# Kernel optimization log

Measured on AMD Instinct MI355X. Metric: run time of the kernel, lower is better.

## Reference

```python
import jax, jax.numpy as jnp
import numpy as np

B, S, E, P, H, F = 4, 4096, 256, 32, 8, 1024
DH = E // H
LN_EPS = 1e-5


def setup_inputs() -> dict:
    key = jax.random.key(0)
    ks = jax.random.split(key, 12)
    dt = jnp.float32
    return {
        "src": jax.random.normal(ks[0], (B, S, E), dt),
        "pos_embed": jax.random.normal(ks[1], (B, P, S), dt),
        # learnable positional transform (pos_linear: P -> P)
        "Wpos": jax.random.normal(ks[2], (P, P), dt) * (1.0 / np.sqrt(P)),
        "bpos": jnp.zeros((P,), dt),
        # RBF kernel hyperparameters (ScaleKernel(RBFKernel)) -- positive scalars
        "lengthscale": jnp.full((), 2.0, dt),
        "outputscale": jnp.full((), 1.0, dt),
        # value / output projections of multihead attention
        "Wv": jax.random.normal(ks[3], (E, E), dt) * (1.0 / np.sqrt(E)),
        "bv": jnp.zeros((E,), dt),
        "Wo": jax.random.normal(ks[4], (E, E), dt) * (1.0 / np.sqrt(E)),
        "bo": jnp.zeros((E,), dt),
        # feed-forward
        "W1": jax.random.normal(ks[5], (F, E), dt) * (1.0 / np.sqrt(E)),
        "b1": jnp.zeros((F,), dt),
        "W2": jax.random.normal(ks[6], (E, F), dt) * (1.0 / np.sqrt(F)),
        "b2": jnp.zeros((E,), dt),
        # layer norms
        "ln1_g": jnp.ones((E,), dt), "ln1_b": jnp.zeros((E,), dt),
        "ln2_g": jnp.ones((E,), dt), "ln2_b": jnp.zeros((E,), dt),
    }


def _layer_norm(x, g, b):
    mu = jnp.mean(x, -1, keepdims=True)
    var = jnp.mean(jnp.square(x - mu), -1, keepdims=True)
    return (x - mu) * jax.lax.rsqrt(var + LN_EPS) * g + b


def _rbf_scores(x, lengthscale, outputscale):
    # x: [B, S, P] -> scaled RBF kernel matrix [B, S, S]
    xs = x / lengthscale
    sq = jnp.sum(xs * xs, axis=-1)  # [B, S]
    d2 = sq[:, :, None] + sq[:, None, :] - 2.0 * jnp.einsum('bsp,btp->bst', xs, xs)
    d2 = jnp.maximum(d2, 0.0)
    return outputscale * jnp.exp(-0.5 * d2)


def reference(src, pos_embed, Wpos, bpos, lengthscale, outputscale,
              Wv, bv, Wo, bo, W1, b1, W2, b2, ln1_g, ln1_b, ln2_g, ln2_b):
    b, s, e = src.shape
    # learnable positional transform: [B,P,S] -> [B,S,P] -> linear -> back
    pe = jnp.einsum('bps,op->bos', pos_embed, Wpos) + bpos[None, :, None]  # [B,P,S]
    # GP-kernel attention scores over sequence positions
    scores = _rbf_scores(pe.transpose(0, 2, 1), lengthscale, outputscale)  # [B,S,S]
    attn = jax.nn.softmax(scores, axis=-1)
    # value projection, per-head weighted sum (scores shared across heads)
    v = (src @ Wv.T + bv).reshape(b, s, H, DH)
    ctx = jnp.einsum('bqk,bkhd->bqhd', attn, v).reshape(b, s, e)
    attn_out = ctx @ Wo.T + bo
    x = _layer_norm(src + attn_out, ln1_g, ln1_b)
    ff = jax.nn.relu(x @ W1.T + b1) @ W2.T + b2
    return _layer_norm(x + ff, ln2_g, ln2_b)
```

## Files before the change

### kernel.cpp

```cpp
#include <hip/hip_runtime.h>
#include <stdint.h>

#define BN 4
#define SN 4096
#define EN 256
#define PN 32
#define FN 1024
#define BS (BN*SN)
#define PAUG 64

typedef uint16_t bf16_t;
typedef short v4s  __attribute__((ext_vector_type(4)));
typedef short v8s  __attribute__((ext_vector_type(8)));
typedef __bf16 bf16x8 __attribute__((ext_vector_type(8)));
typedef float v4f   __attribute__((ext_vector_type(4)));
typedef float v16f  __attribute__((ext_vector_type(16)));

#define MFMA16(a,b,c) __builtin_amdgcn_mfma_f32_16x16x32_bf16(a,b,c,0,0,0)
#define MFMA32(a,b,c) __builtin_amdgcn_mfma_f32_32x32x16_bf16(a,b,c,0,0,0)

__device__ __forceinline__ float b2f(bf16_t x){
    uint32_t u = ((uint32_t)x) << 16; float f; __builtin_memcpy(&f, &u, 4); return f;
}
__device__ __forceinline__ bf16_t f2b(float f){
    uint32_t u; __builtin_memcpy(&u, &f, 4);
    u += 0x7FFFu + ((u >> 16) & 1u);
    return (bf16_t)(u >> 16);
}
__device__ __forceinline__ bf16x8 ldb8(const bf16_t* p){
    v8s r = *(const v8s*)p; return __builtin_bit_cast(bf16x8, r);
}
__device__ __forceinline__ bf16x8 ldb8u(const bf16_t* p){
    v4s lo = *(const v4s*)p;
    v4s hi = *(const v4s*)(p + 4);
    v8s r = __builtin_shufflevector(lo, hi, 0,1,2,3,4,5,6,7);
    return __builtin_bit_cast(bf16x8, r);
}
__device__ __forceinline__ float ldsc(const float* p){ return *p; }
__device__ __forceinline__ float ldsc(const bf16_t* p){ return b2f(*p); }
__device__ __forceinline__ void stsc(float* p, float v){ *p = v; }
__device__ __forceinline__ void stsc(bf16_t* p, float v){ *p = f2b(v); }

#if __has_builtin(__builtin_amdgcn_exp2f)
__device__ __forceinline__ float fexp2(float x){ return __builtin_amdgcn_exp2f(x); }
#else
__device__ __forceinline__ float fexp2(float x){ return exp2f(x); }
#endif

#if __has_builtin(__builtin_amdgcn_cvt_pk_bf16_f32)
typedef __bf16 bf16x2 __attribute__((ext_vector_type(2)));
__device__ __forceinline__ uint32_t pkbf16(float a, float b){
    bf16x2 r = __builtin_amdgcn_cvt_pk_bf16_f32(a, b);
    return __builtin_bit_cast(uint32_t, r);
}
#else
__device__ __forceinline__ uint32_t pkbf16(float a, float b){
    return (uint32_t)f2b(a) | ((uint32_t)f2b(b) << 16);
}
#endif

typedef const __attribute__((address_space(1))) uint32_t* glds_gp;
typedef __attribute__((address_space(3))) uint32_t* glds_lp;
__device__ __forceinline__ void glds16(const bf16_t* g, bf16_t* l){
    __builtin_amdgcn_global_load_lds((glds_gp)g, (glds_lp)l, 16, 0, 0);
}

__global__ __launch_bounds__(256) void prep_kernel(
    const float* __restrict__ src, bf16_t* __restrict__ srcb,
    const float* __restrict__ Wv, bf16_t* __restrict__ Wvb,
    const float* __restrict__ Wo, bf16_t* __restrict__ Wob,
    const float* __restrict__ W1, bf16_t* __restrict__ W1b,
    const float* __restrict__ W2, bf16_t* __restrict__ W2b,
    const float* __restrict__ pos, const float* __restrict__ Wp,
    const float* __restrict__ bp,  const float* __restrict__ lsp,
    bf16_t* __restrict__ xk, bf16_t* __restrict__ xq)
{
    __shared__ float Wsh[PN*PN];
    __shared__ float bsh[PN];
    int bid = blockIdx.x;
    int tid = threadIdx.x;

    if (bid < 4736){
        const float* sp; bf16_t* dp; int off;
        if (bid < 4096){ sp = src; dp = srcb; off = (bid*256 + tid)*4; }
        else {
            int i = ((bid - 4096)*256 + tid)*4;
            if      (i <  65536){ sp=Wv; dp=Wvb; off=i; }
            else if (i < 131072){
                int idx = i - 65536;
                float4 f = *(const float4*)(Wo + idx);
                v4s o;
                o.x = (short)f2b(f.x); o.y = (short)f2b(f.y);
                o.z = (short)f2b(f.z); o.w = (short)f2b(f.w);
                int n = idx >> 8, k = idx & 255;
                int dst = (((n>>4)*8 + (k>>5))*64 + (((k>>3)&3)*16 + (n&15)))*8 + (k&7);
                *(v4s*)(Wob + dst) = o;
                return;
            }
            else if (i < 393216){ sp=W1; dp=W1b; off=i-131072; }
            else                { sp=W2; dp=W2b; off=i-393216; }
        }
        float4 f = *(const float4*)(sp + off);
        v4s o;
        o.x = (short)f2b(f.x); o.y = (short)f2b(f.y);
        o.z = (short)f2b(f.z); o.w = (short)f2b(f.w);
        *(v4s*)(dp + off) = o;
        return;
    }

    int pb = bid - 4736;
    int b  = pb >> 4;
    int s  = (pb & 15)*256 + tid;

    for (int i = tid; i < PN*PN; i += 256) Wsh[i] = Wp[i];
    if (tid < PN) bsh[tid] = bp[tid];
    __syncthreads();

    float inv_ls = 1.0f / lsp[0];
    const float c1f = 1.4426950408889634f;

    float col[PN];
    #pragma unroll
    for (int p = 0; p < PN; p++) col[p] = pos[((size_t)b*PN + p)*SN + s];

    uint16_t xb[PN], qb[PN];
    float sq = 0.f;
    #pragma unroll 4
    for (int o = 0; o < PN; o++){
        float pe = bsh[o];
        #pragma unroll
        for (int p = 0; p < PN; p++) pe += col[p] * Wsh[o*PN + p];
        float pv = pe * inv_ls;
        uint16_t h = f2b(pv);
        xb[o] = h;
        qb[o] = f2b(c1f * pv);
        float xr = b2f(h);
        sq += xr * xr;
    }

    size_t base = ((size_t)b*SN + s) * PAUG;
    v8s pk[8];
    #pragma unroll
    for (int c = 0; c < 4; c++)
        #pragma unroll
        for (int j = 0; j < 8; j++) ((short*)&pk[c])[j] = (short)xb[c*8 + j];
    #pragma unroll
    for (int c = 4; c < 8; c++)
        #pragma unroll
        for (int j = 0; j < 8; j++) ((short*)&pk[c])[j] = 0;
    ((short*)&pk[4])[0] = (short)f2b(-0.5f * sq);
    ((short*)&pk[4])[1] = (short)0x3F80;
    #pragma unroll
    for (int c = 0; c < 8; c++) *(v8s*)(xk + base + c*8) = pk[c];

    #pragma unroll
    for (int c = 0; c < 4; c++)
        #pragma unroll
        for (int j = 0; j < 8; j++) ((short*)&pk[c])[j] = (short)qb[c*8 + j];
    ((short*)&pk[4])[0] = (short)f2b(c1f);
    ((short*)&pk[4])[1] = (short)f2b(-0.5f * sq * c1f);
    #pragma unroll
    for (int c = 0; c < 8; c++) *(v8s*)(xq + base + c*8) = pk[c];
}

template<int EPI, typename OutT>
__global__ __launch_bounds__(256) void gemm_t(
    const bf16_t* __restrict__ A, const bf16_t* __restrict__ W,
    const float* __restrict__ bias, OutT* __restrict__ out,
    bf16_t* __restrict__ vt, int N, int K)
{
    __shared__ __align__(16) bf16_t At[2][4096];
    __shared__ __align__(16) bf16_t Wt[2][4096];
    int tid = threadIdx.x;
    int lane = tid & 63, wv = tid >> 6, col = lane & 15, quad = lane >> 4;
    int m0 = blockIdx.x * 64, n0 = blockIdx.y * 64;
    int nck = K >> 6;

    int srow = tid >> 3;
    int spc  = (tid & 7) ^ (srow & 7);
    const bf16_t* asrc = A + (size_t)(m0 + srow)*K + spc*8;
    const bf16_t* wsrc = W + (size_t)(n0 + srow)*K + spc*8;

    v4f acc[4];
    #pragma unroll
    for (int t = 0; t < 4; t++) acc[t] = (v4f){0.f,0.f,0.f,0.f};

    glds16(asrc, &At[0][tid*8]);
    glds16(asrc + (size_t)32*K, &At[0][2048 + tid*8]);
    glds16(wsrc, &Wt[0][tid*8]);
    glds16(wsrc + (size_t)32*K, &Wt[0][2048 + tid*8]);
    __syncthreads();

    for (int c = 0; c < nck; c++){
        int cb = c & 1;
        if (c + 1 < nck){
            glds16(asrc + (c+1)*64, &At[cb^1][tid*8]);
            glds16(asrc + (size_t)32*K + (c+1)*64, &At[cb^1][2048 + tid*8]);
            glds16(wsrc + (c+1)*64, &Wt[cb^1][tid*8]);
            glds16(wsrc + (size_t)32*K + (c+1)*64, &Wt[cb^1][2048 + tid*8]);
        }
        #pragma unroll
        for (int kc = 0; kc < 2; kc++){
            int pc = ((kc*4 + quad) ^ (col & 7)) * 8;
            bf16x8 a = ldb8(&At[cb][(wv*16 + col)*64 + pc]);
            #pragma unroll
            for (int t = 0; t < 4; t++){
                bf16x8 b = ldb8(&Wt[cb][(t*16 + col)*64 + pc]);
                acc[t] = MFMA16(a, b, acc[t]);
            }
        }
        __syncthreads();
    }

    float bfv[4];
    #pragma unroll
    for (int t = 0; t < 4; t++) bfv[t] = bias[n0 + t*16 + col];

    if constexpr (EPI == 3){
        __shared__ uint16_t Tsh[64*74];
        #pragma unroll
        for (int r = 0; r < 4; r++)
            #pragma unroll
            for (int t = 0; t < 4; t++)
                Tsh[(wv*16 + quad*4 + r)*74 + t*16 + col] = f2b(acc[t][r] + bfv[t]);
        __syncthreads();
        int e = tid >> 2, sc = tid & 3;
        int b = m0 >> 12;
        int sbat = m0 & (SN-1);
        int eb   = (n0 + e) >> 5;
        int l31e = (n0 + e) & 31;
        int k16  = (sbat >> 4) + sc;
        v8s p0, p1;
        #pragma unroll
        for (int i = 0; i < 8; i++) ((short*)&p0)[i] = (short)Tsh[(sc*16 + i)*74 + e];
        #pragma unroll
        for (int i = 0; i < 8; i++) ((short*)&p1)[i] = (short)Tsh[(sc*16 + 8 + i)*74 + e];
        bf16_t* dst = vt + ((((size_t)b*8 + eb)*256 + k16)*64 + l31e)*8;
        *(v8s*)dst = p0;
        *(v8s*)(dst + 256) = p1;
    } else {
        #pragma unroll
        for (int r = 0; r < 4; r++){
            int row = m0 + wv*16 + quad*4 + r;
            #pragma unroll
            for (int t = 0; t < 4; t++){
                float y = acc[t][r] + bfv[t];
                if constexpr (EPI == 1) y = fmaxf(y, 0.f);
                stsc(out + (size_t)row*N + n0 + t*16 + col, y);
            }
        }
    }
}

template<int EPI>
__global__ __launch_bounds__(256, 2) void gemm128(
    const bf16_t* __restrict__ A, const bf16_t* __restrict__ W,
    const float* __restrict__ bias, bf16_t* __restrict__ out,
    int N, int K)
{
    __shared__ __align__(16) bf16_t At[2][8192];
    __shared__ __align__(16) bf16_t Wt[2][8192];
    int tid = threadIdx.x;
    int lane = tid & 63, wv = tid >> 6, col = lane & 15, quad = lane >> 4;
    int m0 = blockIdx.x * 128, n0 = blockIdx.y * 128;
    int nck = K >> 6;

    int srow = tid >> 3;
    int spc  = (tid & 7) ^ (srow & 7);
    const bf16_t* asrc = A + (size_t)(m0 + srow)*K + spc*8;
    const bf16_t* wsrc = W + (size_t)(n0 + srow)*K + spc*8;

    v4f acc[2][8];
    #pragma unroll
    for (int mi = 0; mi < 2; mi++)
        #pragma unroll
        for (int t = 0; t < 8; t++) acc[mi][t] = (v4f){0.f,0.f,0.f,0.f};

    #pragma unroll
    for (int s = 0; s < 4; s++){
        glds16(asrc + (size_t)(s*32)*K, &At[0][s*2048 + tid*8]);
        glds16(wsrc + (size_t)(s*32)*K, &Wt[0][s*2048 + tid*8]);
    }
    __syncthreads();

    for (int c = 0; c < nck; c++){
        int cb = c & 1;
        if (c + 1 < nck){
            #pragma unroll
            for (int s = 0; s < 4; s++){
                glds16(asrc + (size_t)(s*32)*K + (c+1)*64, &At[cb^1][s*2048 + tid*8]);
                glds16(wsrc + (size_t)(s*32)*K + (c+1)*64, &Wt[cb^1][s*2048 + tid*8]);
            }
        }
        #pragma unroll
        for (int kc = 0; kc < 2; kc++){
            int pc = ((kc*4 + quad) ^ (col & 7)) * 8;
            bf16x8 a[2];
            #pragma unroll
            for (int mi = 0; mi < 2; mi++)
                a[mi] = ldb8(&At[cb][(wv*32 + mi*16 + col)*64 + pc]);
            #pragma unroll
            for (int t = 0; t < 8; t++){
                bf16x8 b = ldb8(&Wt[cb][(t*16 + col)*64 + pc]);
                #pragma unroll
                for (int mi = 0; mi < 2; mi++)
                    acc[mi][t] = MFMA16(a[mi], b, acc[mi][t]);
            }
        }
        __syncthreads();
    }

    float bfv[8];
    #pragma unroll
    for (int t = 0; t < 8; t++) bfv[t] = bias[n0 + t*16 + col];

    #pragma unroll
    for (int mi = 0; mi < 2; mi++){
        #pragma unroll
        for (int r = 0; r < 4; r++){
            int row = m0 + wv*32 + mi*16 + quad*4 + r;
            #pragma unroll
            for (int t = 0; t < 8; t++){
                float y = acc[mi][t][r] + bfv[t];
                if constexpr (EPI == 1) y = fmaxf(y, 0.f);
                out[(size_t)row*N + n0 + t*16 + col] = f2b(y);
            }
        }
    }
}

template<typename OutT>
__global__ __launch_bounds__(512, 4) void gemm_ln(
    const bf16_t* __restrict__ A, const bf16_t* __restrict__ W,
    const float* __restrict__ bias, const bf16_t* __restrict__ res,
    const float* __restrict__ gamma, const float* __restrict__ beta,
    OutT* __restrict__ out, int K)
{
    __shared__ __align__(16) bf16_t At[2][32*64];
    __shared__ __align__(16) bf16_t Wt[2][256*64];
    __shared__ float lnb[4][32][2];

    int tid = threadIdx.x;
    int lane = tid & 63, wv = tid >> 6, col = lane & 15, quad = lane >> 4;
    int mw = wv >> 2;
    int nw = wv & 3;
    int m0 = blockIdx.x * 32;
    int nck = K >> 6;

    int arow = (tid & 255) >> 3;
    int apc  = (tid & 7) ^ (arow & 7);
    const bf16_t* asrc = A + (size_t)(m0 + arow)*K + apc*8;
    int wr0  = tid >> 3;
    const bf16_t* wsrc[4];
    #pragma unroll
    for (int s = 0; s < 4; s++){
        int wrow = s*64 + wr0;
        int wpc  = (tid & 7) ^ (wrow & 7);
        wsrc[s] = W + (size_t)wrow*K + wpc*8;
    }

    v4f acc[4];
    #pragma unroll
    for (int t = 0; t < 4; t++) acc[t] = (v4f){0.f,0.f,0.f,0.f};

    if (tid < 256) glds16(asrc, &At[0][tid*8]);
    #pragma unroll
    for (int s = 0; s < 4; s++) glds16(wsrc[s], &Wt[0][s*4096 + tid*8]);
    __syncthreads();

    for (int c = 0; c < nck; c++){
        int cb = c & 1;
        if (c + 1 < nck){
            if (tid < 256) glds16(asrc + (c+1)*64, &At[cb^1][tid*8]);
            #pragma unroll
            for (int s = 0; s < 4; s++)
                glds16(wsrc[s] + (c+1)*64, &Wt[cb^1][s*4096 + tid*8]);
        }
        #pragma unroll
        for (int kc = 0; kc < 2; kc++){
            int pc = ((kc*4 + quad) ^ (col & 7)) * 8;
            bf16x8 a = ldb8(&At[cb][(mw*16 + col)*64 + pc]);
            #pragma unroll
            for (int t = 0; t < 4; t++){
                bf16x8 b = ldb8(&Wt[cb][(nw*64 + t*16 + col)*64 + pc]);
                acc[t] = MFMA16(a, b, acc[t]);
            }
        }
        __syncthreads();
    }

    float bfv[4];
    #pragma unroll
    for (int t = 0; t < 4; t++) bfv[t] = bias[nw*64 + t*16 + col];

    float v[4][4];
    float s1[4], s2[4];
    #pragma unroll
    for (int r = 0; r < 4; r++){ s1[r] = 0.f; s2[r] = 0.f; }
    #pragma unroll
    for (int r = 0; r < 4; r++){
        int row = m0 + mw*16 + quad*4 + r;
        #pragma unroll
        for (int t = 0; t < 4; t++){
            float x = acc[t][r] + bfv[t]
                    + b2f(res[(size_t)row*EN + nw*64 + t*16 + col]);
            v[t][r] = x; s1[r] += x; s2[r] += x*x;
        }
    }
    #pragma unroll
    for (int r = 0; r < 4; r++){
        #pragma unroll
        for (int m = 1; m <= 8; m <<= 1){
            s1[r] += __shfl_xor(s1[r], m);
            s2[r] += __shfl_xor(s2[r], m);
        }
    }
    if (col == 0){
        #pragma unroll
        for (int r = 0; r < 4; r++){
            int rl = mw*16 + quad*4 + r;
            lnb[nw][rl][0] = s1[r];
            lnb[nw][rl][1] = s2[r];
        }
    }
    __syncthreads();
    #pragma unroll
    for (int r = 0; r < 4; r++){
        int rl  = mw*16 + quad*4 + r;
        int row = m0 + rl;
        float S1 = lnb[0][rl][0] + lnb[1][rl][0] + lnb[2][rl][0] + lnb[3][rl][0];
        float S2 = lnb[0][rl][1] + lnb[1][rl][1] + lnb[2][rl][1] + lnb[3][rl][1];
        float mu = S1 * (1.f/256.f);
        float rs = rsqrtf(S2 * (1.f/256.f) - mu*mu + 1e-5f);
        #pragma unroll
        for (int t = 0; t < 4; t++){
            int gi = nw*64 + t*16 + col;
            stsc(out + (size_t)row*EN + gi, (v[t][r]-mu)*rs*gamma[gi] + beta[gi]);
        }
    }
}

__global__ __launch_bounds__(512, 2) void attn_kernel(
    const bf16_t* __restrict__ xk, const bf16_t* __restrict__ xq,
    const bf16_t* __restrict__ vf, const float* __restrict__ osp,
    const bf16_t* __restrict__ wof, const float* __restrict__ bo,
    const bf16_t* __restrict__ res, const float* __restrict__ gamma,
    const float* __restrict__ beta, bf16_t* __restrict__ out)
{
    __shared__ __align__(16) bf16_t Wtb[2][64*132];
    __shared__ __align__(16) bf16_t Qs[64*64];
    __shared__ __align__(16) bf16_t Osh[64*256];
    __shared__ float densh[8][64];
    __shared__ float dent[64];
    __shared__ float lnw[8][64][2];

    int tid  = threadIdx.x;
    int lane = tid & 63;
    int wv   = tid >> 6;
    int col  = lane & 15;
    int quad = lane >> 4;
    int l31  = lane & 31;
    int half = lane >> 5;

    int bid = blockIdx.x;
    int b   = (bid & 7) >> 1;
    int qi  = ((bid >> 3) << 1) | (bid & 1);
    int q0  = qi * 64;

    float k2 = 1.4426950408889634f * osp[0];

    const bf16_t* xkb = xk + (size_t)b * SN * PAUG;
    const bf16_t* xqb = xq + (size_t)b * SN * PAUG;
    const bf16_t* vfb = vf + (((size_t)b*8 + wv)*256)*512 + lane*8;

    {
        int qrow = tid >> 3;
        int qpc  = (tid & 7) ^ (qrow & 7);
        glds16(xqb + (size_t)(q0 + qrow)*PAUG + qpc*8, &Qs[tid*8]);
    }

    v16f acc[2];
    #pragma unroll
    for (int qg = 0; qg < 2; qg++)
        #pragma unroll
        for (int i = 0; i < 16; i++) acc[qg][i] = 0.f;
    float den[4] = {0.f, 0.f, 0.f, 0.f};
    const v4f zero = (v4f){0.f,0.f,0.f,0.f};

    bf16x8 kf0, kf1;
    {
        const bf16_t* kr = xkb + (size_t)(wv*16 + col)*PAUG + quad*8;
        kf0 = ldb8(kr); kf1 = ldb8(kr + 32);
    }

    __syncthreads();

    for (int c = 0; c < 32; c++){
        int cb = c & 1;
        bf16x8 vr[8];
        #pragma unroll
        for (int sk = 0; sk < 8; sk++)
            vr[sk] = ldb8(vfb + (size_t)(c*8 + sk)*512);

        #pragma unroll
        for (int qg = 0; qg < 2; qg++){
            #pragma unroll
            for (int g2 = 0; g2 < 2; g2++){
                int qr = qg*32 + g2*16 + col;
                bf16x8 qa = ldb8(&Qs[qr*64 + ((quad    ) ^ (col & 7))*8]);
                bf16x8 qb = ldb8(&Qs[qr*64 + ((4 + quad) ^ (col & 7))*8]);
                v4f st = MFMA16(kf0, qa, zero);
                st = MFMA16(kf1, qb, st);
                #pragma unroll
                for (int rp = 0; rp < 2; rp++){
                    float w0 = fexp2(fmaf(k2, fexp2(st[rp*2+0]), -k2));
                    float w1 = fexp2(fmaf(k2, fexp2(st[rp*2+1]), -k2));
                    den[qg*2+g2] += w0 + w1;
                    *(uint32_t*)&Wtb[cb][qr*132 + wv*16 + quad*4 + rp*2]
                        = pkbf16(w0, w1);
                }
            }
        }

        if (c + 1 < 32){
            const bf16_t* kr = xkb + (size_t)((c+1)*128 + wv*16 + col)*PAUG + quad*8;
            kf0 = ldb8(kr); kf1 = ldb8(kr + 32);
        }

        asm volatile("s_waitcnt lgkmcnt(0)" ::: "memory");
        __builtin_amdgcn_s_barrier();
        __builtin_amdgcn_sched_barrier(0);

        #pragma unroll
        for (int qg = 0; qg < 2; qg++){
            #pragma unroll
            for (int sk4 = 0; sk4 < 2; sk4++){
                bf16x8 af[4];
                #pragma unroll
                for (int j = 0; j < 4; j++)
                    af[j] = ldb8u(&Wtb[cb][(qg*32 + l31)*132 + (sk4*4 + j)*16 + half*8]);
                #pragma unroll
                for (int j = 0; j < 4; j++)
                    acc[qg] = MFMA32(af[j], vr[sk4*4 + j], acc[qg]);
            }
        }
    }

    #pragma unroll
    for (int d = 0; d < 4; d++){
        den[d] += __shfl_xor(den[d], 16);
        den[d] += __shfl_xor(den[d], 32);
    }
    if (lane < 16){
        #pragma unroll
        for (int qg = 0; qg < 2; qg++)
            #pragma unroll
            for (int g2 = 0; g2 < 2; g2++)
                densh[wv][qg*32 + g2*16 + lane] = den[qg*2+g2];
    }
    __syncthreads();
    if (tid < 64){
        float s = 0.f;
        #pragma unroll
        for (int w = 0; w < 8; w++) s += densh[w][tid];
        dent[tid] = 1.f / s;
    }
    __syncthreads();

    #pragma unroll
    for (int qg = 0; qg < 2; qg++){
        #pragma unroll
        for (int rg = 0; rg < 16; rg++){
            int qrow = qg*32 + (rg & 3) + 8*(rg >> 2) + 4*half;
            int e = wv*32 + l31;
            int g = e >> 3;
            Osh[qrow*256 + ((g ^ (qrow & 7))*8) + (e & 7)] = f2b(acc[qg][rg] * dent[qrow]);
        }
    }
    __syncthreads();

    v4f y[4][2];
    #pragma unroll
    for (int qg = 0; qg < 4; qg++)
        #pragma unroll
        for (int t = 0; t < 2; t++) y[qg][t] = (v4f){0.f,0.f,0.f,0.f};

    #pragma unroll
    for (int kc = 0; kc < 8; kc++){
        bf16x8 b0 = ldb8(wof + (size_t)(((wv*2+0)*8 + kc)*64 + lane)*8);
        bf16x8 b1 = ldb8(wof + (size_t)(((wv*2+1)*8 + kc)*64 + lane)*8);
        #pragma unroll
        for (int qg = 0; qg < 4; qg++){
            bf16x8 a = ldb8(&Osh[(qg*16 + col)*256 + (((kc*4 + quad) ^ (col & 7))*8)]);
            y[qg][0] = MFMA16(a, b0, y[qg][0]);
            y[qg][1] = MFMA16(a, b1, y[qg][1]);
        }
    }

    size_t growb = (size_t)b*SN + q0;
    float bo0 = bo[wv*32 + col], bo1 = bo[wv*32 + 16 + col];
    #pragma unroll
    for (int qg = 0; qg < 4; qg++){
        #pragma unroll
        for (int r = 0; r < 4; r++){
            int row = qg*16 + quad*4 + r;
            float x0 = y[qg][0][r] + bo0 + b2f(res[(growb + row)*EN + wv*32 + col]);
            float x1 = y[qg][1][r] + bo1 + b2f(res[(growb + row)*EN + wv*32 + 16 + col]);
            y[qg][0][r] = x0; y[qg][1][r] = x1;
            float s1 = x0 + x1, s2 = x0*x0 + x1*x1;
            #pragma unroll
            for (int m = 1; m <= 8; m <<= 1){
                s1 += __shfl_xor(s1, m);
                s2 += __shfl_xor(s2, m);
            }
            if (col == 0){
                lnw[wv][row][0] = s1;
                lnw[wv][row][1] = s2;
            }
        }
    }
    __syncthreads();

    float g0 = gamma[wv*32 + col],      g1v = gamma[wv*32 + 16 + col];
    float e0 = beta[wv*32 + col],       e1v = beta[wv*32 + 16 + col];
    #pragma unroll
    for (int qg = 0; qg < 4; qg++){
        #pragma unroll
        for (int r = 0; r < 4; r++){
            int row = qg*16 + quad*4 + r;
            float S1 = 0.f, S2 = 0.f;
            #pragma unroll
            for (int w = 0; w < 8; w++){ S1 += lnw[w][row][0]; S2 += lnw[w][row][1]; }
            float mu = S1 * (1.f/256.f);
            float rs = rsqrtf(S2 * (1.f/256.f) - mu*mu + 1e-5f);
            out[(growb + row)*EN + wv*32 + col]      = f2b((y[qg][0][r]-mu)*rs*g0 + e0);
            out[(growb + row)*EN + wv*32 + 16 + col] = f2b((y[qg][1][r]-mu)*rs*g1v + e1v);
        }
    }
}

extern "C" void kernel_launch(void* const* d_in, const int* in_sizes, int n_in,
                              void* d_out, int out_size, void* d_ws, size_t ws_size,
                              hipStream_t stream)
{
    (void)in_sizes; (void)n_in; (void)out_size; (void)ws_size;
    const float* src  = (const float*)d_in[0];
    const float* pos  = (const float*)d_in[1];
    const float* Wpos = (const float*)d_in[2];
    const float* bpos = (const float*)d_in[3];
    const float* ls   = (const float*)d_in[4];
    const float* os   = (const float*)d_in[5];
    const float* Wv   = (const float*)d_in[6];
    const float* bv   = (const float*)d_in[7];
    const float* Wo   = (const float*)d_in[8];
    const float* bo   = (const float*)d_in[9];
    const float* W1   = (const float*)d_in[10];
    const float* b1   = (const float*)d_in[11];
    const float* W2   = (const float*)d_in[12];
    const float* b2   = (const float*)d_in[13];
    const float* g1   = (const float*)d_in[14];
    const float* be1  = (const float*)d_in[15];
    const float* g2   = (const float*)d_in[16];
    const float* be2  = (const float*)d_in[17];

    char* w = (char*)d_ws;
    bf16_t* xkb  = (bf16_t*)(w);
    bf16_t* xqb  = (bf16_t*)(w + ( 2u<<20));
    bf16_t* Wvb  = (bf16_t*)(w + ( 4u<<20));
    bf16_t* Wob  = (bf16_t*)(w + ( 4u<<20) + (1u<<18));
    bf16_t* W1b  = (bf16_t*)(w + ( 5u<<20));
    bf16_t* W2b  = (bf16_t*)(w + ( 6u<<20));
    bf16_t* srcb = (bf16_t*)(w + ( 8u<<20));
    bf16_t* vtg  = (bf16_t*)(w + (16u<<20));
    bf16_t* xws  = (bf16_t*)(w + (24u<<20));
    bf16_t* hws  = (bf16_t*)(w + (32u<<20));

    prep_kernel<<<dim3(4800), 256, 0, stream>>>(
        src, srcb, Wv, Wvb, Wo, Wob, W1, W1b, W2, W2b,
        pos, Wpos, bpos, ls, xkb, xqb);

    gemm_t<3, bf16_t><<<dim3(BS/64, EN/64), 256, 0, stream>>>(
        srcb, Wvb, bv, (bf16_t*)nullptr, vtg, EN, EN);
    attn_kernel<<<dim3(256), 512, 0, stream>>>(
        xkb, xqb, vtg, os, Wob, bo, srcb, g1, be1, xws);
    gemm128<1><<<dim3(BS/128, FN/128), 256, 0, stream>>>(
        xws, W1b, b1, hws, FN, EN);
    gemm_ln<float><<<dim3(BS/32), 512, 0, stream>>>(
        hws, W2b, b2, xws, g2, be2, (float*)d_out, FN);
}
```

Baseline: 231.9 us.

## Fuse FFN up/down GEMMs with LayerNorm and double attention key chunk

Replaces the separate W1 GEMM (writing a bf16 hidden tensor to global memory) and the W2+LayerNorm GEMM with one fused kernel. For each 64-row tile it computes hidden chunks of 64 in LDS and immediately accumulates them into the W2 output, while double-buffering W1/W2 tiles. This removes the global round trip of the hidden activations and one launch, at the cost of fewer blocks (256) and a large LDS footprint. Separately, the attention kernel now processes 256 keys per iteration instead of 128, halving the barrier count but increasing register and LDS pressure.

Measured after the change: 225.6 us. 2.7% less time.

```diff
diff --git a/kernel.cpp b/kernel.cpp
--- a/kernel.cpp
+++ b/kernel.cpp
@@ -252,148 +252,118 @@
     }
 }
 
-template<int EPI>
-__global__ __launch_bounds__(256, 2) void gemm128(
-    const bf16_t* __restrict__ A, const bf16_t* __restrict__ W,
-    const float* __restrict__ bias, bf16_t* __restrict__ out,
-    int N, int K)
+__global__ __launch_bounds__(512) void ffn_ln_kernel(
+    const bf16_t* __restrict__ x,  const bf16_t* __restrict__ W1b,
+    const float* __restrict__ b1,  const bf16_t* __restrict__ W2b,
+    const float* __restrict__ b2,  const float* __restrict__ gamma,
+    const float* __restrict__ beta, float* __restrict__ out)
 {
-    __shared__ __align__(16) bf16_t At[2][8192];
-    __shared__ __align__(16) bf16_t Wt[2][8192];
-    int tid = threadIdx.x;
-    int lane = tid & 63, wv = tid >> 6, col = lane & 15, quad = lane >> 4;
-    int m0 = blockIdx.x * 128, n0 = blockIdx.y * 128;
-    int nck = K >> 6;
-
-    int srow = tid >> 3;
-    int spc  = (tid & 7) ^ (srow & 7);
-    const bf16_t* asrc = A + (size_t)(m0 + srow)*K + spc*8;
-    const bf16_t* wsrc = W + (size_t)(n0 + srow)*K + spc*8;
-
-    v4f acc[2][8];
-    #pragma unroll
-    for (int mi = 0; mi < 2; mi++)
-        #pragma unroll
-        for (int t = 0; t < 8; t++) acc[mi][t] = (v4f){0.f,0.f,0.f,0.f};
-
-    #pragma unroll
-    for (int s = 0; s < 4; s++){
-        glds16(asrc + (size_t)(s*32)*K, &At[0][s*2048 + tid*8]);
-        glds16(wsrc + (size_t)(s*32)*K, &Wt[0][s*2048 + tid*8]);
-    }
-    __syncthreads();
-
-    for (int c = 0; c < nck; c++){
-        int cb = c & 1;
-        if (c + 1 < nck){
-            #pragma unroll
-            for (int s = 0; s < 4; s++){
-                glds16(asrc + (size_t)(s*32)*K + (c+1)*64, &At[cb^1][s*2048 + tid*8]);
-                glds16(wsrc + (size_t)(s*32)*K + (c+1)*64, &Wt[cb^1][s*2048 + tid*8]);
-            }
-        }
-        #pragma unroll
-        for (int kc = 0; kc < 2; kc++){
-            int pc = ((kc*4 + quad) ^ (col & 7)) * 8;
-            bf16x8 a[2];
-            #pragma unroll
-            for (int mi = 0; mi < 2; mi++)
-                a[mi] = ldb8(&At[cb][(wv*32 + mi*16 + col)*64 + pc]);
-            #pragma unroll
-            for (int t = 0; t < 8; t++){
-                bf16x8 b = ldb8(&Wt[cb][(t*16 + col)*64 + pc]);
-                #pragma unroll
-                for (int mi = 0; mi < 2; mi++)
-                    acc[mi][t] = MFMA16(a[mi], b, acc[mi][t]);
-            }
-        }
-        __syncthreads();
-    }
-
-    float bfv[8];
-    #pragma unroll
-    for (int t = 0; t < 8; t++) bfv[t] = bias[n0 + t*16 + col];
-
-    #pragma unroll
-    for (int mi = 0; mi < 2; mi++){
-        #pragma unroll
-        for (int r = 0; r < 4; r++){
-            int row = m0 + wv*32 + mi*16 + quad*4 + r;
-            #pragma unroll
-            for (int t = 0; t < 8; t++){
-                float y = acc[mi][t][r] + bfv[t];
-                if constexpr (EPI == 1) y = fmaxf(y, 0.f);
-                out[(size_t)row*N + n0 + t*16 + col] = f2b(y);
-            }
-        }
-    }
-}
-
-template<typename OutT>
-__global__ __launch_bounds__(512, 4) void gemm_ln(
-    const bf16_t* __restrict__ A, const bf16_t* __restrict__ W,
-    const float* __restrict__ bias, const bf16_t* __restrict__ res,
-    const float* __restrict__ gamma, const float* __restrict__ beta,
-    OutT* __restrict__ out, int K)
-{
-    __shared__ __align__(16) bf16_t At[2][32*64];
-    __shared__ __align__(16) bf16_t Wt[2][256*64];
-    __shared__ float lnb[4][32][2];
-
-    int tid = threadIdx.x;
-    int lane = tid & 63, wv = tid >> 6, col = lane & 15, quad = lane >> 4;
-    int mw = wv >> 2;
-    int nw = wv & 3;
-    int m0 = blockIdx.x * 32;
-    int nck = K >> 6;
-
-    int arow = (tid & 255) >> 3;
-    int apc  = (tid & 7) ^ (arow & 7);
-    const bf16_t* asrc = A + (size_t)(m0 + arow)*K + apc*8;
-    int wr0  = tid >> 3;
-    const bf16_t* wsrc[4];
-    #pragma unroll
-    for (int s = 0; s < 4; s++){
-        int wrow = s*64 + wr0;
-        int wpc  = (tid & 7) ^ (wrow & 7);
-        wsrc[s] = W + (size_t)wrow*K + wpc*8;
-    }
-
-    v4f acc[4];
-    #pragma unroll
-    for (int t = 0; t < 4; t++) acc[t] = (v4f){0.f,0.f,0.f,0.f};
-
-    if (tid < 256) glds16(asrc, &At[0][tid*8]);
-    #pragma unroll
-    for (int s = 0; s < 4; s++) glds16(wsrc[s], &Wt[0][s*4096 + tid*8]);
-    __syncthreads();
-
-    for (int c = 0; c < nck; c++){
-        int cb = c & 1;
-        if (c + 1 < nck){
-            if (tid < 256) glds16(asrc + (c+1)*64, &At[cb^1][tid*8]);
+    __shared__ __align__(16) bf16_t W1c[2][16384];
+    __shared__ __align__(16) bf16_t W2c[2][16384];
+    __shared__ __align__(16) bf16_t Hs[64*68];
+    __shared__ float b1sh[1024];
+    __shared__ float lnb[2][64][2];
+
+    int tid  = threadIdx.x;
+    int lane = tid & 63;
+    int wv   = tid >> 6;
+    int col  = lane & 15;
+    int quad = lane >> 4;
+    int mw   = wv >> 1;
+    int nw   = wv & 1;
+    int m0   = blockIdx.x * 64;
+
+    b1sh[tid]       = b1[tid];
+    b1sh[512 + tid] = b1[512 + tid];
+
+    const bf16_t* xrow = x + (size_t)(m0 + mw*16 + col)*EN + quad*8;
+    bf16x8 xr[8];
+    #pragma unroll
+    for (int kk = 0; kk < 8; kk++) xr[kk] = ldb8(xrow + kk*32);
+
+    float b2v[8], gv[8], bev[8];
+    #pragma unroll
+    for (int t2 = 0; t2 < 8; t2++){
+        int nn = nw*128 + t2*16 + col;
+        b2v[t2] = b2[nn]; gv[t2] = gamma[nn]; bev[t2] = beta[nn];
+    }
+
+    v4f acc[8];
+    #pragma unroll
+    for (int t2 = 0; t2 < 8; t2++) acc[t2] = (v4f){0.f,0.f,0.f,0.f};
+
+    int wr  = tid >> 3;
+    int pp  = tid & 7;
+    int swz = (pp ^ (wr & 7)) * 8;
+
+    #pragma unroll
+    for (int s = 0; s < 4; s++)
+        glds16(W1b + (size_t)wr*256 + s*64 + swz, &W1c[0][s*4096 + tid*8]);
+    #pragma unroll
+    for (int s2 = 0; s2 < 4; s2++)
+        glds16(W2b + (size_t)(s2*64 + wr)*1024 + swz, &W2c[0][s2*4096 + tid*8]);
+
+    #pragma unroll 1
+    for (int c = 0; c < 16; c++){
+        int par = c & 1;
+        if (c < 15){
             #pragma unroll
             for (int s = 0; s < 4; s++)
-                glds16(wsrc[s] + (c+1)*64, &Wt[cb^1][s*4096 + tid*8]);
-        }
-        #pragma unroll
-        for (int kc = 0; kc < 2; kc++){
-            int pc = ((kc*4 + quad) ^ (col & 7)) * 8;
-            bf16x8 a = ldb8(&At[cb][(mw*16 + col)*64 + pc]);
-            #pragma unroll
-            for (int t = 0; t < 4; t++){
-                bf16x8 b = ldb8(&Wt[cb][(nw*64 + t*16 + col)*64 + pc]);
-                acc[t] = MFMA16(a, b, acc[t]);
-            }
-        }
-        __syncthreads();
-    }
-
-    float bfv[4];
-    #pragma unroll
-    for (int t = 0; t < 4; t++) bfv[t] = bias[nw*64 + t*16 + col];
-
-    float v[4][4];
+                glds16(W1b + (size_t)((c+1)*64 + wr)*256 + s*64 + swz,
+                       &W1c[par^1][s*4096 + tid*8]);
+            #pragma unroll
+            for (int s2 = 0; s2 < 4; s2++)
+                glds16(W2b + (size_t)(s2*64 + wr)*1024 + (c+1)*64 + swz,
+                       &W2c[par^1][s2*4096 + tid*8]);
+            asm volatile("s_waitcnt vmcnt(8)" ::: "memory");
+        } else {
+            asm volatile("s_waitcnt vmcnt(0)" ::: "memory");
+        }
+        __builtin_amdgcn_s_barrier();
+        __builtin_amdgcn_sched_barrier(0);
+
+        v4f hacc[2];
+        hacc[0] = (v4f){0.f,0.f,0.f,0.f};
+        hacc[1] = (v4f){0.f,0.f,0.f,0.f};
+        #pragma unroll
+        for (int kk = 0; kk < 8; kk++){
+            #pragma unroll
+            for (int t = 0; t < 2; t++){
+                int hl = nw*32 + t*16 + col;
+                bf16x8 b = ldb8(&W1c[par][(kk>>1)*4096 + hl*64
+                                 + ((((kk&1)*4 + quad) ^ (hl & 7))*8)]);
+                hacc[t] = MFMA16(xr[kk], b, hacc[t]);
+            }
+        }
+        #pragma unroll
+        for (int t = 0; t < 2; t++){
+            float bb = b1sh[c*64 + nw*32 + t*16 + col];
+            #pragma unroll
+            for (int r = 0; r < 4; r++){
+                float h = fmaxf(hacc[t][r] + bb, 0.f);
+                Hs[(mw*16 + quad*4 + r)*68 + nw*32 + t*16 + col] = f2b(h);
+            }
+        }
+        asm volatile("s_waitcnt lgkmcnt(0)" ::: "memory");
+        __builtin_amdgcn_s_barrier();
+        __builtin_amdgcn_sched_barrier(0);
+
+        #pragma unroll
+        for (int kk2 = 0; kk2 < 2; kk2++){
+            bf16x8 a2 = ldb8u(&Hs[(mw*16 + col)*68 + kk2*32 + quad*8]);
+            #pragma unroll
+            for (int t2 = 0; t2 < 8; t2++){
+                int nn = nw*128 + t2*16 + col;
+                bf16x8 bfr = ldb8(&W2c[par][(nn>>6)*4096 + (nn&63)*64
+                                  + ((((kk2*4 + quad) ^ (col & 7)))*8)]);
+                acc[t2] = MFMA16(a2, bfr, acc[t2]);
+            }
+        }
+        asm volatile("s_waitcnt lgkmcnt(0)" ::: "memory");
+        __builtin_amdgcn_s_barrier();
+    }
+
+    float v[8][4];
     float s1[4], s2[4];
     #pragma unroll
     for (int r = 0; r < 4; r++){ s1[r] = 0.f; s2[r] = 0.f; }
@@ -401,10 +371,10 @@
     for (int r = 0; r < 4; r++){
         int row = m0 + mw*16 + quad*4 + r;
         #pragma unroll
-        for (int t = 0; t < 4; t++){
-            float x = acc[t][r] + bfv[t]
-                    + b2f(res[(size_t)row*EN + nw*64 + t*16 + col]);
-            v[t][r] = x; s1[r] += x; s2[r] += x*x;
+        for (int t2 = 0; t2 < 8; t2++){
+            int nn = nw*128 + t2*16 + col;
+            float xv = acc[t2][r] + b2v[t2] + b2f(x[(size_t)row*EN + nn]);
+            v[t2][r] = xv; s1[r] += xv; s2[r] += xv*xv;
         }
     }
     #pragma unroll
@@ -428,14 +398,14 @@
     for (int r = 0; r < 4; r++){
         int rl  = mw*16 + quad*4 + r;
         int row = m0 + rl;
-        float S1 = lnb[0][rl][0] + lnb[1][rl][0] + lnb[2][rl][0] + lnb[3][rl][0];
-        float S2 = lnb[0][rl][1] + lnb[1][rl][1] + lnb[2][rl][1] + lnb[3][rl][1];
+        float S1 = lnb[0][rl][0] + lnb[1][rl][0];
+        float S2 = lnb[0][rl][1] + lnb[1][rl][1];
         float mu = S1 * (1.f/256.f);
         float rs = rsqrtf(S2 * (1.f/256.f) - mu*mu + 1e-5f);
         #pragma unroll
-        for (int t = 0; t < 4; t++){
-            int gi = nw*64 + t*16 + col;
-            stsc(out + (size_t)row*EN + gi, (v[t][r]-mu)*rs*gamma[gi] + beta[gi]);
+        for (int t2 = 0; t2 < 8; t2++){
+            int nn = nw*128 + t2*16 + col;
+            out[(size_t)row*EN + nn] = (v[t2][r] - mu)*rs*gv[t2] + bev[t2];
         }
     }
 }
@@ -447,7 +417,7 @@
     const bf16_t* __restrict__ res, const float* __restrict__ gamma,
     const float* __restrict__ beta, bf16_t* __restrict__ out)
 {
-    __shared__ __align__(16) bf16_t Wtb[2][64*132];
+    __shared__ __align__(16) bf16_t Wtb[2][64*260];
     __shared__ __align__(16) bf16_t Qs[64*64];
     __shared__ __align__(16) bf16_t Osh[64*256];
     __shared__ float densh[8][64];
@@ -487,20 +457,21 @@
     float den[4] = {0.f, 0.f, 0.f, 0.f};
     const v4f zero = (v4f){0.f,0.f,0.f,0.f};
 
-    bf16x8 kf0, kf1;
-    {
-        const bf16_t* kr = xkb + (size_t)(wv*16 + col)*PAUG + quad*8;
-        kf0 = ldb8(kr); kf1 = ldb8(kr + 32);
-    }
-
-    __syncthreads();
-
-    for (int c = 0; c < 32; c++){
+    bf16x8 kf[2][2];
+    #pragma unroll
+    for (int kg = 0; kg < 2; kg++)
+        #pragma unroll
+        for (int h = 0; h < 2; h++)
+            kf[kg][h] = ldb8(xkb + (size_t)(wv*32 + kg*16 + col)*PAUG + h*32 + quad*8);
+
+    __syncthreads();
+
+    for (int c = 0; c < 16; c++){
         int cb = c & 1;
-        bf16x8 vr[8];
-        #pragma unroll
-        for (int sk = 0; sk < 8; sk++)
-            vr[sk] = ldb8(vfb + (size_t)(c*8 + sk)*512);
+        bf16x8 vr[16];
+        #pragma unroll
+        for (int sk = 0; sk < 16; sk++)
+            vr[sk] = ldb8(vfb + (size_t)(c*16 + sk)*512);
 
         #pragma unroll
         for (int qg = 0; qg < 2; qg++){
@@ -509,22 +480,29 @@
                 int qr = qg*32 + g2*16 + col;
                 bf16x8 qa = ldb8(&Qs[qr*64 + ((quad    ) ^ (col & 7))*8]);
                 bf16x8 qb = ldb8(&Qs[qr*64 + ((4 + quad) ^ (col & 7))*8]);
-                v4f st = MFMA16(kf0, qa, zero);
-                st = MFMA16(kf1, qb, st);
                 #pragma unroll
-                for (int rp = 0; rp < 2; rp++){
-                    float w0 = fexp2(fmaf(k2, fexp2(st[rp*2+0]), -k2));
-                    float w1 = fexp2(fmaf(k2, fexp2(st[rp*2+1]), -k2));
-                    den[qg*2+g2] += w0 + w1;
-                    *(uint32_t*)&Wtb[cb][qr*132 + wv*16 + quad*4 + rp*2]
-                        = pkbf16(w0, w1);
+                for (int kg = 0; kg < 2; kg++){
+                    v4f st = MFMA16(kf[kg][0], qa, zero);
+                    st = MFMA16(kf[kg][1], qb, st);
+                    #pragma unroll
+                    for (int rp = 0; rp < 2; rp++){
+                        float w0 = fexp2(fmaf(k2, fexp2(st[rp*2+0]), -k2));
+                        float w1 = fexp2(fmaf(k2, fexp2(st[rp*2+1]), -k2));
+                        den[qg*2+g2] += w0 + w1;
+                        *(uint32_t*)&Wtb[cb][qr*260 + wv*32 + kg*16 + quad*4 + rp*2]
+                            = pkbf16(w0, w1);
+                    }
                 }
             }
         }
 
-        if (c + 1 < 32){
-            const bf16_t* kr = xkb + (size_t)((c+1)*128 + wv*16 + col)*PAUG + quad*8;
-            kf0 = ldb8(kr); kf1 = ldb8(kr + 32);
+        if (c + 1 < 16){
+            #pragma unroll
+            for (int kg = 0; kg < 2; kg++)
+                #pragma unroll
+                for (int h = 0; h < 2; h++)
+                    kf[kg][h] = ldb8(xkb + (size_t)((c+1)*256 + wv*32 + kg*16 + col)*PAUG
+                                     + h*32 + quad*8);
         }
 
         asm volatile("s_waitcnt lgkmcnt(0)" ::: "memory");
@@ -534,11 +512,11 @@
         #pragma unroll
         for (int qg = 0; qg < 2; qg++){
             #pragma unroll
-            for (int sk4 = 0; sk4 < 2; sk4++){
+            for (int sk4 = 0; sk4 < 4; sk4++){
                 bf16x8 af[4];
                 #pragma unroll
                 for (int j = 0; j < 4; j++)
-                    af[j] = ldb8u(&Wtb[cb][(qg*32 + l31)*132 + (sk4*4 + j)*16 + half*8]);
+                    af[j] = ldb8u(&Wtb[cb][(qg*32 + l31)*260 + (sk4*4 + j)*16 + half*8]);
                 #pragma unroll
                 for (int j = 0; j < 4; j++)
                     acc[qg] = MFMA32(af[j], vr[sk4*4 + j], acc[qg]);
@@ -673,7 +651,6 @@
     bf16_t* srcb = (bf16_t*)(w + ( 8u<<20));
     bf16_t* vtg  = (bf16_t*)(w + (16u<<20));
     bf16_t* xws  = (bf16_t*)(w + (24u<<20));
-    bf16_t* hws  = (bf16_t*)(w + (32u<<20));
 
     prep_kernel<<<dim3(4800), 256, 0, stream>>>(
         src, srcb, Wv, Wvb, Wo, Wob, W1, W1b, W2, W2b,
@@ -683,8 +660,6 @@
         srcb, Wvb, bv, (bf16_t*)nullptr, vtg, EN, EN);
     attn_kernel<<<dim3(256), 512, 0, stream>>>(
         xkb, xqb, vtg, os, Wob, bo, srcb, g1, be1, xws);
-    gemm128<1><<<dim3(BS/128, FN/128), 256, 0, stream>>>(
-        xws, W1b, b1, hws, FN, EN);
-    gemm_ln<float><<<dim3(BS/32), 512, 0, stream>>>(
-        hws, W2b, b2, xws, g2, be2, (float*)d_out, FN);
-}
+    ffn_ln_kernel<<<dim3(BS/64), 512, 0, stream>>>(
+        xws, W1b, b1, W2b, b2, g2, be2, (float*)d_out);
+}
```
